# Optimization experiments

Hardware: AMD Instinct MI355X
Metric: run time of the kernel (lower is better)

Reference implementation:

```python
import jax, jax.numpy as jnp
import numpy as np

B, TI, TO = 32, 128, 64
VI, VO = 32000, 32000
E, H, A = 256, 512, 512
EOS, BOS = 0, 1


def setup_inputs() -> dict:
    key = jax.random.key(0)
    ks = jax.random.split(key, 24)
    def p(k, shape):
        return jax.random.normal(k, shape, jnp.float32) * 0.05
    return {
        "inp": jax.random.randint(ks[0], (B, TI), 0, VI),
        "out": jax.random.randint(ks[1], (B, TO), 0, VO),
        "emb_inp": p(ks[2], (VI, E)),
        "emb_out": p(ks[3], (VO, E)),
        "enc_Wih_f": p(ks[4], (3 * H, E)),
        "enc_Whh_f": p(ks[5], (3 * H, H)),
        "enc_bih_f": p(ks[6], (3 * H,)),
        "enc_bhh_f": p(ks[7], (3 * H,)),
        "enc_Wih_b": p(ks[8], (3 * H, E)),
        "enc_Whh_b": p(ks[9], (3 * H, H)),
        "enc_bih_b": p(ks[10], (3 * H,)),
        "enc_bhh_b": p(ks[11], (3 * H,)),
        "dec_start_W": p(ks[12], (H, 2 * H)),
        "dec_start_b": p(ks[13], (H,)),
        "dec_Wih": p(ks[14], (3 * H, E + 2 * H)),
        "dec_Whh": p(ks[15], (3 * H, H)),
        "dec_bih": p(ks[16], (3 * H,)),
        "dec_bhh": p(ks[17], (3 * H,)),
        "attn_Wenc": p(ks[18], (A, 2 * H)),
        "attn_benc": p(ks[19], (A,)),
        "attn_Wdec": p(ks[20], (A, H)),
        "attn_bdec": p(ks[21], (A,)),
        "attn_v": p(ks[22], (A,)),
        "attn_vb": jnp.zeros((), jnp.float32),
        "logits_W": p(ks[23], (VO, 3 * H)),
        "logits_b": jnp.zeros((VO,), jnp.float32),
    }


def _gru_dir(x, Wih, bih, Whh, bhh, reverse):
    # x: [B,T,E]; precompute input projections once: [B,T,3H]
    xp = jnp.einsum('bte,ge->btg', x, Wih) + bih
    Hd = Whh.shape[1]
    def step(h, xt):
        gh = h @ Whh.T + bhh
        xr, xz, xn = jnp.split(xt, 3, -1)
        hr, hz, hn = jnp.split(gh, 3, -1)
        r = jax.nn.sigmoid(xr + hr)
        z = jax.nn.sigmoid(xz + hz)
        n = jnp.tanh(xn + r * hn)
        h_new = (1.0 - z) * n + z * h
        return h_new, h_new
    h0 = jnp.zeros((x.shape[0], Hd), x.dtype)
    _, hs = jax.lax.scan(step, h0, jnp.swapaxes(xp, 0, 1), reverse=reverse)
    return jnp.swapaxes(hs, 0, 1)  # [B,T,H]


def _forward(inp, out, emb_inp, emb_out,
             enc_Wih_f, enc_Whh_f, enc_bih_f, enc_bhh_f,
             enc_Wih_b, enc_Whh_b, enc_bih_b, enc_bhh_b,
             dec_start_W, dec_start_b, dec_Wih, dec_Whh, dec_bih, dec_bhh,
             attn_Wenc, attn_benc, attn_Wdec, attn_bdec, attn_v, attn_vb,
             logits_W, logits_b):
    x = emb_inp[inp]  # [B,TI,E]
    ef = _gru_dir(x, enc_Wih_f, enc_bih_f, enc_Whh_f, enc_bhh_f, False)
    eb = _gru_dir(x, enc_Wih_b, enc_bih_b, enc_Whh_b, enc_bhh_b, True)
    enc = jnp.concatenate([ef, eb], -1)  # [B,TI,2H]
    mask = (inp != EOS).astype(jnp.float32)
    lengths = jnp.minimum(mask.sum(1).astype(jnp.int32), TI - 1)
    last = enc[jnp.arange(enc.shape[0]), lengths]  # [B,2H]
    dec0 = last @ dec_start_W.T + dec_start_b  # [B,H]
    enc_proj = jnp.einsum('btd,ad->bta', enc, attn_Wenc) + attn_benc  # [B,TI,A]

    def attend(dec):
        dp = dec @ attn_Wdec.T + attn_bdec  # [B,A]
        s = jnp.tanh(enc_proj + dp[:, None, :]) @ attn_v + attn_vb  # [B,TI]
        s = jnp.where(mask > 0, s, -jnp.inf)
        pr = jax.nn.softmax(s, -1)
        return jnp.einsum('bt,btd->bd', pr, enc), pr

    a0, _ = attend(dec0)

    def step(carry, tok):
        h, a = carry
        e = emb_out[tok]  # [B,E]
        xg = jnp.concatenate([e, a], -1) @ dec_Wih.T + dec_bih
        hg = h @ dec_Whh.T + dec_bhh
        xr, xz, xn = jnp.split(xg, 3, -1)
        hr, hz, hn = jnp.split(hg, 3, -1)
        r = jax.nn.sigmoid(xr + hr)
        z = jax.nn.sigmoid(xz + hz)
        n = jnp.tanh(xn + r * hn)
        h_new = (1.0 - z) * n + z * h
        a_new, _ = attend(h_new)
        lg = jnp.concatenate([h_new, a_new], -1) @ logits_W.T + logits_b
        return (h_new, a_new), lg

    toks = jnp.swapaxes(out[:, :-1], 0, 1)  # [TO-1, B]
    _, lgs = jax.lax.scan(step, (dec0, a0), toks)  # [TO-1,B,VO]
    first = jnp.log(jax.nn.one_hot(jnp.full((out.shape[0],), BOS), VO) + 1e-9)
    return jnp.swapaxes(jnp.concatenate([first[None], lgs], 0), 0, 1)  # [B,TO,VO]


def reference(inp, out, emb_inp, emb_out,
              enc_Wih_f, enc_Whh_f, enc_bih_f, enc_bhh_f,
              enc_Wih_b, enc_Whh_b, enc_bih_b, enc_bhh_b,
              dec_start_W, dec_start_b, dec_Wih, dec_Whh, dec_bih, dec_bhh,
              attn_Wenc, attn_benc, attn_Wdec, attn_bdec, attn_v, attn_vb,
              logits_W, logits_b):
    return _forward(inp, out, emb_inp, emb_out,
                    enc_Wih_f, enc_Whh_f, enc_bih_f, enc_bhh_f,
                    enc_Wih_b, enc_Whh_b, enc_bih_b, enc_bhh_b,
                    dec_start_W, dec_start_b, dec_Wih, dec_Whh, dec_bih, dec_bhh,
                    attn_Wenc, attn_benc, attn_Wdec, attn_bdec, attn_v, attn_vb,
                    logits_W, logits_b)
```

## Files before the change

kernel.cpp:

```cpp
#include <hip/hip_runtime.h>
#include <math.h>
#include <stdint.h>

#define B_   32
#define TI_  128
#define TO_  64
#define E_   256
#define H_   512
#define A_   512
#define VO_  32000
#define G3_  1536
#define D2H_ 1024

using short8 = __attribute__((ext_vector_type(8))) short;
using f32x4  = __attribute__((ext_vector_type(4))) float;
typedef __attribute__((ext_vector_type(2))) __bf16 bf16x2_t;

__device__ __forceinline__ unsigned short f2bf(float x) {
  uint32_t u = __builtin_bit_cast(uint32_t, x);
  uint32_t r = (u + 0x7fffu + ((u >> 16) & 1u)) >> 16;
  return (unsigned short)r;
}
__device__ __forceinline__ uint32_t pack2(float lo, float hi) {
  return (uint32_t)f2bf(lo) | ((uint32_t)f2bf(hi) << 16);
}
__device__ __forceinline__ float bflo(uint32_t u) { return __builtin_bit_cast(float, u << 16); }
__device__ __forceinline__ float bfhi(uint32_t u) { return __builtin_bit_cast(float, u & 0xffff0000u); }

#if __has_builtin(__builtin_amdgcn_fdot2_f32_bf16)
__device__ __forceinline__ float dot2bf(uint32_t a, uint32_t b, float c) {
  return __builtin_amdgcn_fdot2_f32_bf16(__builtin_bit_cast(bf16x2_t, a),
                                         __builtin_bit_cast(bf16x2_t, b), c, false);
}
#else
__device__ __forceinline__ float dot2bf(uint32_t a, uint32_t b, float c) {
  return fmaf(bfhi(a), bfhi(b), fmaf(bflo(a), bflo(b), c));
}
#endif

__device__ __forceinline__ float sigf(float x) {
  return __builtin_amdgcn_rcpf(1.f + __expf(-x));
}
__device__ __forceinline__ float tanhf_(float x) {
  return fmaf(-2.f, __builtin_amdgcn_rcpf(1.f + __expf(2.f * x)), 1.f);
}

__global__ __launch_bounds__(256) void k_init(unsigned short* __restrict__ tail) {
  int i = blockIdx.x * 256 + threadIdx.x;
  if (i < 32 * G3_) tail[i] = 0;
}

__global__ __launch_bounds__(256) void k_cvt_bf16(const float* __restrict__ in,
                                                  unsigned short* __restrict__ out, int n8) {
  int i = blockIdx.x * 256 + threadIdx.x;
  if (i >= n8) return;
  float4 a = ((const float4*)in)[2 * i];
  float4 b = ((const float4*)in)[2 * i + 1];
  uint4 o = { pack2(a.x, a.y), pack2(a.z, a.w), pack2(b.x, b.y), pack2(b.z, b.w) };
  ((uint4*)out)[i] = o;
}

__global__ __launch_bounds__(256) void k_cvt_multi(
    const float* __restrict__ i0, unsigned short* __restrict__ o0,
    const float* __restrict__ i1, unsigned short* __restrict__ o1,
    const float* __restrict__ i2, unsigned short* __restrict__ o2,
    const float* __restrict__ i3, unsigned short* __restrict__ o3) {
  int u = blockIdx.x * 256 + threadIdx.x;
  const float* in; unsigned short* out; int lu;
  if      (u < 245760) { in = i0; out = o0; lu = u; }
  else if (u < 311296) { in = i1; out = o1; lu = u - 245760; }
  else if (u < 360448) { in = i2; out = o2; lu = u - 311296; }
  else if (u < 409600) { in = i3; out = o3; lu = u - 360448; }
  else return;
  float4 a = ((const float4*)in)[2 * lu];
  float4 b = ((const float4*)in)[2 * lu + 1];
  uint4 o = { pack2(a.x, a.y), pack2(a.z, a.w), pack2(b.x, b.y), pack2(b.z, b.w) };
  ((uint4*)out)[lu] = o;
}

__global__ __launch_bounds__(256) void k_cvt_tp(
    const float* __restrict__ i0, uint32_t* __restrict__ o0,
    const float* __restrict__ i1, uint32_t* __restrict__ o1,
    const float* __restrict__ i2, uint32_t* __restrict__ o2,
    const float* __restrict__ i3, uint32_t* __restrict__ o3) {
  int u = blockIdx.x * 256 + threadIdx.x;
  const float* in; uint32_t* out; int lu, N;
  if      (u < 393216)  { in = i0; out = o0; lu = u;          N = 1536; }
  else if (u < 786432)  { in = i1; out = o1; lu = u - 393216; N = 1536; }
  else if (u < 1179648) { in = i2; out = o2; lu = u - 786432; N = 1536; }
  else if (u < 1310720) { in = i3; out = o3; lu = u - 1179648; N = 512; }
  else return;
  int c = lu % N, kp = lu / N;
  const float* p = in + (size_t)c * 512 + 2 * kp;
  out[lu] = pack2(p[0], p[1]);
}

__global__ __launch_bounds__(256) void k_packT(const unsigned short* __restrict__ encWA,
                                               uint32_t* __restrict__ EWPd) {
  int idx = blockIdx.x * 256 + threadIdx.x;
  if (idx >= 32 * 64 * 1536) return;
  int g = idx % 1536, q = idx / 1536;
  int b = q >> 6, tp = q & 63;
  size_t r0 = ((size_t)(b * 128 + 2 * tp)) * 1536 + g;
  EWPd[idx] = (uint32_t)encWA[r0] | ((uint32_t)encWA[r0 + 1536] << 16);
}

__global__ __launch_bounds__(256) void k_gather_xb(const int* __restrict__ inp,
                                                   const float* __restrict__ emb,
                                                   unsigned short* __restrict__ xb) {
  int idx = blockIdx.x * 256 + threadIdx.x;
  if (idx >= 4096 * 32) return;
  int row = idx >> 5, e8 = idx & 31;
  int tok = inp[row];
  const float4* s = (const float4*)(emb + (size_t)tok * E_ + e8 * 8);
  float4 a = s[0], b = s[1];
  uint4 o = { pack2(a.x, a.y), pack2(a.z, a.w), pack2(b.x, b.y), pack2(b.z, b.w) };
  ((uint4*)xb)[idx] = o;
}

__global__ __launch_bounds__(256) void k_gather_xeb(const int* __restrict__ outi,
                                                    const float* __restrict__ emb,
                                                    unsigned short* __restrict__ xeb) {
  int idx = blockIdx.x * 256 + threadIdx.x;
  if (idx >= 2016 * 32) return;
  int row = idx >> 5, e8 = idx & 31;
  int i = row >> 5, b = row & 31;
  int tok = outi[b * TO_ + i];
  const float4* s = (const float4*)(emb + (size_t)tok * E_ + e8 * 8);
  float4 a = s[0], bb = s[1];
  uint4 o = { pack2(a.x, a.y), pack2(a.z, a.w), pack2(bb.x, bb.y), pack2(bb.z, bb.w) };
  ((uint4*)xeb)[idx] = o;
}

__global__ __launch_bounds__(256) void k_first(float* __restrict__ dout) {
  int idx = blockIdx.x * 256 + threadIdx.x;
  if (idx >= B_ * VO_) return;
  int b = idx / VO_, v = idx % VO_;
  dout[(size_t)b * TO_ * VO_ + v] = (v == 1) ? 0.f : -20.72326583694641f;
}

template <int MODE>
__global__ __launch_bounds__(256) void k_bgemm(
    const unsigned short* __restrict__ A, int lda,
    const unsigned short* __restrict__ Bt, int ldb,
    const float* __restrict__ bias,
    void* __restrict__ Cv, int ldc, int M, int N, int K) {
  __shared__ alignas(16) unsigned short As[128 * 32];
  __shared__ alignas(16) unsigned short Bs[128 * 32];
  const int tid = threadIdx.x;
  const int wave = tid >> 6, lane = tid & 63;
  const int m0 = blockIdx.y * 128, n0 = blockIdx.x * 128;
  const int wr = wave >> 1, wc = wave & 1;

  f32x4 acc[4][4];
#pragma unroll
  for (int i = 0; i < 4; ++i)
#pragma unroll
    for (int j = 0; j < 4; ++j) acc[i][j] = (f32x4){0.f, 0.f, 0.f, 0.f};

  const int srow = tid >> 2;
  const int sbyte = (tid & 3) * 16;
  const int fr = lane & 15;
  const int fkb = (lane >> 4) * 16;

  for (int k0 = 0; k0 < K; k0 += 32) {
#pragma unroll
    for (int rd = 0; rd < 2; ++rd) {
      int row = rd * 64 + srow;
      int ra = min(m0 + row, M - 1);
      const char* ga = (const char*)(A + (size_t)ra * lda + k0) + sbyte;
      const char* gb = (const char*)(Bt + (size_t)(n0 + row) * ldb + k0) + sbyte;
      __builtin_amdgcn_global_load_lds(
          (const __attribute__((address_space(1))) uint32_t*)ga,
          (__attribute__((address_space(3))) uint32_t*)((char*)As + rd * 4096 + wave * 1024),
          16, 0, 0);
      __builtin_amdgcn_global_load_lds(
          (const __attribute__((address_space(1))) uint32_t*)gb,
          (__attribute__((address_space(3))) uint32_t*)((char*)Bs + rd * 4096 + wave * 1024),
          16, 0, 0);
    }
    __syncthreads();

    short8 af[4], bf[4];
#pragma unroll
    for (int i = 0; i < 4; ++i) {
      int ar = wr * 64 + i * 16 + fr;
      int bc = wc * 64 + i * 16 + fr;
      af[i] = *(const short8*)((const char*)As + ar * 64 + fkb);
      bf[i] = *(const short8*)((const char*)Bs + bc * 64 + fkb);
    }
#pragma unroll
    for (int i = 0; i < 4; ++i)
#pragma unroll
      for (int j = 0; j < 4; ++j)
        acc[i][j] = __builtin_amdgcn_mfma_f32_16x16x32_bf16(af[i], bf[j], acc[i][j], 0, 0, 0);
    __syncthreads();
  }

  const int crow = (lane >> 4) * 4, ccol = lane & 15;
#pragma unroll
  for (int i = 0; i < 4; ++i) {
#pragma unroll
    for (int r = 0; r < 4; ++r) {
      int m = m0 + wr * 64 + i * 16 + crow + r;
      if (m >= M) continue;
#pragma unroll
      for (int j = 0; j < 4; ++j) {
        int n = n0 + wc * 64 + j * 16 + ccol;
        float v = acc[i][j][r] + (bias ? bias[n] : 0.f);
        if (MODE == 0) {
          ((float*)Cv)[(size_t)m * ldc + n] = v;
        } else if (MODE == 1) {
          ((unsigned short*)Cv)[(size_t)m * ldc + n] = f2bf(v);
        } else {
          int bb = m & 31, st = m >> 5;
          ((float*)Cv)[((size_t)bb * TO_ + st + 1) * VO_ + n] = v;
        }
      }
    }
  }
}

__global__ __launch_bounds__(1024, 4) void k_encoder(
    const unsigned short* __restrict__ xpb_f, const unsigned short* __restrict__ xpb_b,
    const uint32_t* __restrict__ EWPf, const float* __restrict__ bhh_f,
    const uint32_t* __restrict__ EWPb, const float* __restrict__ bhh_b,
    unsigned short* __restrict__ encb) {
  __shared__ uint32_t xrow[768];
  __shared__ float hf[512];
  __shared__ uint32_t hb2[256];
  const int bid = blockIdx.x;
  const int dir = bid >> 5, b = bid & 31;
  const unsigned short* xpb = dir ? xpb_b : xpb_f;
  const uint32_t* EWP = dir ? EWPb : EWPf;
  const float* bhh = dir ? bhh_b : bhh_f;
  const int tid = threadIdx.x;
  const int col = tid >> 1, kh = tid & 1;

  if (tid < 512) hf[tid] = 0.f;
  if (tid < 256) hb2[tid] = 0u;
  float br = 0.f, bz = 0.f, bn = 0.f;
  if (kh == 0) { br = bhh[col]; bz = bhh[512 + col]; bn = bhh[1024 + col]; }
  uint32_t* encw = (uint32_t*)encb;

  for (int t = 0; t < TI_; ++t) {
    const int tt = dir ? (TI_ - 1 - t) : t;
    const uint32_t* xr = (const uint32_t*)(xpb + (size_t)(b * 128 + tt) * G3_);
    if (tid < 768) xrow[tid] = xr[tid];
    __syncthreads();

    float ar = 0.f, az = 0.f, an = 0.f;
    const uint32_t* wp = EWP + (size_t)(kh * 128) * 1536 + col;
#pragma unroll 8
    for (int k = 0; k < 128; ++k) {
      uint32_t hv = hb2[kh * 128 + k];
      ar = dot2bf(hv, wp[0], ar);
      az = dot2bf(hv, wp[512], az);
      an = dot2bf(hv, wp[1024], an);
      wp += 1536;
    }
    ar += __shfl_xor(ar, 1);
    az += __shfl_xor(az, 1);
    an += __shfl_xor(an, 1);

    float hnew = 0.f;
    if (kh == 0) {
      uint32_t ur = xrow[col >> 1], uz = xrow[256 + (col >> 1)], un = xrow[512 + (col >> 1)];
      float xrv = (col & 1) ? bfhi(ur) : bflo(ur);
      float xzv = (col & 1) ? bfhi(uz) : bflo(uz);
      float xnv = (col & 1) ? bfhi(un) : bflo(un);
      float r = sigf(xrv + ar + br);
      float z = sigf(xzv + az + bz);
      float n = tanhf_(xnv + r * (an + bn));
      hnew = (1.f - z) * n + z * hf[col];
    }
    __syncthreads();
    float hnb = __shfl_down(hnew, 2);
    if ((tid & 3) == 0)
      encw[(size_t)(b * 128 + tt) * 512 + dir * 256 + (tid >> 2)] = pack2(hnew, hnb);
    if (kh == 0) hf[col] = hnew;
    __syncthreads();
    if (tid < 256) hb2[tid] = pack2(hf[2 * tid], hf[2 * tid + 1]);
    __syncthreads();
  }
}

__global__ __launch_bounds__(1024, 4) void k_decoder(
    const int* __restrict__ inp,
    const unsigned short* __restrict__ encb,
    const unsigned short* __restrict__ encpb,
    const float* __restrict__ XE,
    const uint32_t* __restrict__ EWPd,
    const uint32_t* __restrict__ WHPd,
    const uint32_t* __restrict__ WDPd,
    const float* __restrict__ dsW, const float* __restrict__ dsb,
    const float* __restrict__ dbhh,
    const float* __restrict__ abdec, const float* __restrict__ abenc,
    const float* __restrict__ av, const float* __restrict__ avb,
    unsigned short* __restrict__ HAb) {
  __shared__ float hf[512];
  __shared__ uint32_t hb2[256];
  __shared__ uint32_t prb2[64];
  __shared__ float pr[128];
  __shared__ float sc[128];
  __shared__ float msk[128];
  __shared__ float dp[512];
  __shared__ float vavf[512];
  __shared__ float red[1024];
  __shared__ float red2[1024];
  __shared__ float dpx[4];
  const int b = blockIdx.x, tid = threadIdx.x;
  const int col = tid >> 1, kh = tid & 1;

  float db_r = 0.f, db_z = 0.f, db_n = 0.f, adb = 0.f;
  if (kh == 0) {
    db_r = dbhh[col]; db_z = dbhh[512 + col]; db_n = dbhh[1024 + col];
    adb = abdec[col] + abenc[col];
  }
  const float avb0 = avb[0];

  if (tid < 128) msk[tid] = (inp[b * TI_ + tid] != 0) ? 1.f : 0.f;
  if (tid < 512) vavf[tid] = av[tid];
  __syncthreads();
  if (tid < 64) {
    float s = msk[tid] + msk[tid + 64];
#pragma unroll
    for (int o = 32; o > 0; o >>= 1) s += __shfl_xor(s, o);
    if (tid == 0) dpx[0] = s;
  }
  __syncthreads();
  const int len = min((int)dpx[0], TI_ - 1);

  if (tid < 512) {
    uint32_t u = ((const uint32_t*)encb)[(size_t)(b * 128 + len) * 512 + tid];
    red[2 * tid] = bflo(u);
    red[2 * tid + 1] = bfhi(u);
  }
  __syncthreads();
  {
    const float4* w = (const float4*)(dsW + (size_t)col * D2H_ + kh * 512);
    float acc = 0.f;
#pragma unroll 8
    for (int k = 0; k < 128; ++k) {
      float4 l = ((const float4*)red)[kh * 128 + k];
      float4 q = w[k];
      acc = fmaf(l.x, q.x, fmaf(l.y, q.y, fmaf(l.z, q.z, fmaf(l.w, q.w, acc))));
    }
    acc += __shfl_xor(acc, 1);
    __syncthreads();
    if (kh == 0) hf[col] = acc + dsb[col];
    __syncthreads();
    if (tid < 256) hb2[tid] = pack2(hf[2 * tid], hf[2 * tid + 1]);
    __syncthreads();
  }

  auto attend = [&](int step) {
    {
      const uint32_t* wp = WDPd + (size_t)(kh * 128) * 512 + col;
      float d_ = 0.f;
#pragma unroll 8
      for (int k = 0; k < 128; ++k) {
        d_ = dot2bf(hb2[kh * 128 + k], wp[0], d_);
        wp += 512;
      }
      d_ += __shfl_xor(d_, 1);
      if (kh == 0) dp[col] = d_ + adb;
    }
    __syncthreads();
    {
      int t = tid >> 3, s8 = tid & 7;
      const uint32_t* ep = (const uint32_t*)encpb + (size_t)(b * 128 + t) * 256 + s8;
      float s = 0.f;
#pragma unroll 4
      for (int i = 0; i < 32; ++i) {
        int j = s8 + 8 * i;
        uint32_t u = ep[8 * i];
        float2 d2 = *(const float2*)&dp[2 * j];
        float2 v2 = *(const float2*)&vavf[2 * j];
        s = fmaf(v2.x, tanhf_(bflo(u) + d2.x), s);
        s = fmaf(v2.y, tanhf_(bfhi(u) + d2.y), s);
      }
      s += __shfl_xor(s, 1);
      s += __shfl_xor(s, 2);
      s += __shfl_xor(s, 4);
      if (s8 == 0) sc[t] = s;
    }
    __syncthreads();
    if (tid < 128) sc[tid] = (msk[tid] > 0.f) ? sc[tid] + avb0 : -1e30f;
    __syncthreads();
    if (tid < 64) {
      float m = fmaxf(sc[tid], sc[tid + 64]);
#pragma unroll
      for (int o = 32; o > 0; o >>= 1) m = fmaxf(m, __shfl_xor(m, o));
      if (tid == 0) dpx[1] = m;
    }
    __syncthreads();
    if (tid < 128) pr[tid] = __expf(sc[tid] - dpx[1]);
    __syncthreads();
    if (tid < 64) {
      float s2 = pr[tid] + pr[tid + 64];
#pragma unroll
      for (int o = 32; o > 0; o >>= 1) s2 += __shfl_xor(s2, o);
      if (tid == 0) dpx[2] = s2;
    }
    __syncthreads();
    float inv = __builtin_amdgcn_rcpf(dpx[2]);
    if (tid < 128) pr[tid] *= inv;
    __syncthreads();
    if (tid < 64) prb2[tid] = pack2(pr[2 * tid], pr[2 * tid + 1]);
    if (step >= 0) {
      const uint32_t* eb = (const uint32_t*)encb + (size_t)b * 128 * 512;
      int d = tid & 511, tq = tid >> 9;
      float x0 = 0.f, x1 = 0.f;
#pragma unroll 4
      for (int k = 0; k < 64; ++k) {
        int t = tq * 64 + k;
        float p = pr[t];
        uint32_t u = eb[(size_t)t * 512 + d];
        x0 = fmaf(p, bflo(u), x0);
        x1 = fmaf(p, bfhi(u), x1);
      }
      red[tid] = x0; red2[tid] = x1;
      __syncthreads();
      if (tid < 512) {
        x0 = red[tid] + red[tid + 512];
        x1 = red2[tid] + red2[tid + 512];
        uint32_t* hrow = (uint32_t*)(HAb + ((size_t)step * 32 + b) * G3_);
        hrow[256 + tid] = pack2(x0, x1);
      }
    }
    __syncthreads();
  };

  auto gru = [&](int i) {
    float xr_ = 0.f, xz_ = 0.f, xn_ = 0.f, hr_ = 0.f, hz_ = 0.f, hn_ = 0.f;
    {
      const uint32_t* ew = EWPd + ((size_t)b * 64 + kh * 32) * 1536 + col;
#pragma unroll 8
      for (int k = 0; k < 32; ++k) {
        uint32_t pv = prb2[kh * 32 + k];
        xr_ = dot2bf(pv, ew[0], xr_);
        xz_ = dot2bf(pv, ew[512], xz_);
        xn_ = dot2bf(pv, ew[1024], xn_);
        ew += 1536;
      }
    }
    {
      const uint32_t* wp = WHPd + (size_t)(kh * 128) * 1536 + col;
#pragma unroll 8
      for (int k = 0; k < 128; ++k) {
        uint32_t hv = hb2[kh * 128 + k];
        hr_ = dot2bf(hv, wp[0], hr_);
        hz_ = dot2bf(hv, wp[512], hz_);
        hn_ = dot2bf(hv, wp[1024], hn_);
        wp += 1536;
      }
    }
    float t_r = xr_ + hr_; t_r += __shfl_xor(t_r, 1);
    float t_z = xz_ + hz_; t_z += __shfl_xor(t_z, 1);
    xn_ += __shfl_xor(xn_, 1);
    hn_ += __shfl_xor(hn_, 1);

    float hnew = 0.f;
    if (kh == 0) {
      const float* xrow = XE + ((size_t)i * 32 + b) * G3_;
      float r = sigf(xrow[col] + t_r + db_r);
      float z = sigf(xrow[512 + col] + t_z + db_z);
      float n = tanhf_(xrow[1024 + col] + xn_ + r * (hn_ + db_n));
      hnew = (1.f - z) * n + z * hf[col];
    }
    __syncthreads();
    float hnb = __shfl_down(hnew, 2);
    if ((tid & 3) == 0)
      ((uint32_t*)(HAb + ((size_t)i * 32 + b) * G3_))[tid >> 2] = pack2(hnew, hnb);
    if (kh == 0) hf[col] = hnew;
    __syncthreads();
    if (tid < 256) hb2[tid] = pack2(hf[2 * tid], hf[2 * tid + 1]);
    __syncthreads();
  };

  attend(-1);
  for (int i = 0; i < 63; ++i) {
    gru(i);
    attend(i);
  }
}


extern "C" void kernel_launch(void* const* d_in, const int* in_sizes, int n_in,
                              void* d_out, int out_size, void* d_ws, size_t ws_size,
                              hipStream_t stream) {
  const int*   inp     = (const int*)d_in[0];
  const int*   outi    = (const int*)d_in[1];
  const float* emb_inp = (const float*)d_in[2];
  const float* emb_out = (const float*)d_in[3];
  const float* eWih_f  = (const float*)d_in[4];
  const float* eWhh_f  = (const float*)d_in[5];
  const float* ebih_f  = (const float*)d_in[6];
  const float* ebhh_f  = (const float*)d_in[7];
  const float* eWih_b  = (const float*)d_in[8];
  const float* eWhh_b  = (const float*)d_in[9];
  const float* ebih_b  = (const float*)d_in[10];
  const float* ebhh_b  = (const float*)d_in[11];
  const float* dsW     = (const float*)d_in[12];
  const float* dsb     = (const float*)d_in[13];
  const float* dWih    = (const float*)d_in[14];
  const float* dWhh    = (const float*)d_in[15];
  const float* dbih    = (const float*)d_in[16];
  const float* dbhh    = (const float*)d_in[17];
  const float* aWenc   = (const float*)d_in[18];
  const float* abenc   = (const float*)d_in[19];
  const float* aWdec   = (const float*)d_in[20];
  const float* abdec   = (const float*)d_in[21];
  const float* av      = (const float*)d_in[22];
  const float* avb     = (const float*)d_in[23];
  const float* lW      = (const float*)d_in[24];
  const float* lb      = (const float*)d_in[25];
  float* dout = (float*)d_out;

  char* ws = (char*)d_ws;
  size_t off = 0;
  auto alloc = [&](size_t bytes) {
    void* p = ws + off;
    off += (bytes + 255) & ~(size_t)255;
    return p;
  };
  unsigned short* xb      = (unsigned short*)alloc((size_t)4096 * 256 * 2);
  unsigned short* xeb     = (unsigned short*)alloc((size_t)2016 * 256 * 2);
  unsigned short* xpb_f   = (unsigned short*)alloc((size_t)4096 * G3_ * 2);
  unsigned short* xpb_b   = (unsigned short*)alloc((size_t)4096 * G3_ * 2);
  unsigned short* encb    = (unsigned short*)alloc((size_t)4096 * D2H_ * 2);
  unsigned short* encpb   = (unsigned short*)alloc((size_t)4096 * 512 * 2);
  unsigned short* encWA   = (unsigned short*)alloc((size_t)4096 * G3_ * 2);
  uint32_t*       EWPd    = (uint32_t*)alloc((size_t)32 * 64 * 1536 * 4);
  float*          XE      = (float*)alloc((size_t)2016 * G3_ * 4);
  unsigned short* HAb     = (unsigned short*)alloc((size_t)2048 * G3_ * 2);
  unsigned short* lWb     = (unsigned short*)alloc((size_t)VO_ * G3_ * 2);
  uint32_t*       EWPf    = (uint32_t*)alloc((size_t)256 * 1536 * 4);
  uint32_t*       EWPb    = (uint32_t*)alloc((size_t)256 * 1536 * 4);
  uint32_t*       WHPd    = (uint32_t*)alloc((size_t)256 * 1536 * 4);
  uint32_t*       WDPd    = (uint32_t*)alloc((size_t)256 * 512 * 4);
  unsigned short* dWihb   = (unsigned short*)alloc((size_t)G3_ * 1280 * 2);
  unsigned short* aWencb  = (unsigned short*)alloc((size_t)512 * D2H_ * 2);
  unsigned short* eWihb_f = (unsigned short*)alloc((size_t)G3_ * 256 * 2);
  unsigned short* eWihb_b = (unsigned short*)alloc((size_t)G3_ * 256 * 2);

  k_init<<<192, 256, 0, stream>>>(HAb + (size_t)2016 * G3_);
  k_cvt_multi<<<1600, 256, 0, stream>>>(dWih, dWihb, aWenc, aWencb,
                                        eWih_f, eWihb_f, eWih_b, eWihb_b);
  k_cvt_tp<<<5120, 256, 0, stream>>>(eWhh_f, EWPf, eWhh_b, EWPb, dWhh, WHPd, aWdec, WDPd);
  k_cvt_bf16<<<24000, 256, 0, stream>>>(lW, lWb, VO_ * G3_ / 8);

  k_gather_xb<<<512, 256, 0, stream>>>(inp, emb_inp, xb);
  k_gather_xeb<<<252, 256, 0, stream>>>(outi, emb_out, xeb);

  {
    dim3 g(12, 32);
    k_bgemm<1><<<g, 256, 0, stream>>>(xb, 256, eWihb_f, 256, ebih_f, xpb_f, G3_, 4096, G3_, 256);
    k_bgemm<1><<<g, 256, 0, stream>>>(xb, 256, eWihb_b, 256, ebih_b, xpb_b, G3_, 4096, G3_, 256);
  }

  k_encoder<<<64, 1024, 0, stream>>>(xpb_f, xpb_b, EWPf, ebhh_f, EWPb, ebhh_b, encb);

  {
    dim3 g(4, 32);
    k_bgemm<1><<<g, 256, 0, stream>>>(encb, D2H_, aWencb, D2H_, nullptr, encpb, 512, 4096, 512, D2H_);
  }
  {
    dim3 g(12, 32);
    k_bgemm<1><<<g, 256, 0, stream>>>(encb, D2H_, dWihb + 256, 1280, nullptr, encWA, G3_, 4096, G3_, D2H_);
  }
  k_packT<<<12288, 256, 0, stream>>>(encWA, EWPd);

  {
    dim3 g(12, 16);
    k_bgemm<0><<<g, 256, 0, stream>>>(xeb, 256, dWihb, 1280, dbih, XE, G3_, 2016, G3_, 256);
  }

  k_decoder<<<32, 1024, 0, stream>>>(inp, encb, encpb, XE, EWPd, WHPd, WDPd,
                                     dsW, dsb, dbhh, abdec, abenc, av, avb, HAb);

  {
    dim3 g(250, 16);
    k_bgemm<3><<<g, 256, 0, stream>>>(HAb, G3_, lWb, G3_, lb, dout, 0, 2016, VO_, G3_);
  }
  k_first<<<4000, 256, 0, stream>>>(dout);
}
```

Measured before the change: 11.10 ms.

## Repack recurrent GRU weights as column pairs with 4-way k-split and register prefetch

Recurrent weight matrices for the encoder and decoder (Whh, attention Wdec, and the per-batch encoder-attention projection) are repacked so each uint2 holds two output columns for a k-pair. Each thread now computes two columns over a quarter of k, with double-buffered register prefetch of weight loads. The hidden state is kept in padded shared memory, so the separate bf16 repack pass and one barrier per step are dropped. The aim is wider global loads and better latency hiding in the latency-bound sequential loops, at the cost of more registers and an extra shuffle reduction stage.

```diff
diff --git a/kernel.cpp b/kernel.cpp
--- a/kernel.cpp
+++ b/kernel.cpp
@@ -78,31 +78,41 @@
   ((uint4*)out)[lu] = o;
 }
 
-__global__ __launch_bounds__(256) void k_cvt_tp(
-    const float* __restrict__ i0, uint32_t* __restrict__ o0,
-    const float* __restrict__ i1, uint32_t* __restrict__ o1,
-    const float* __restrict__ i2, uint32_t* __restrict__ o2,
-    const float* __restrict__ i3, uint32_t* __restrict__ o3) {
+__global__ __launch_bounds__(256) void k_cvt_w2(
+    const float* __restrict__ i0, uint2* __restrict__ o0,
+    const float* __restrict__ i1, uint2* __restrict__ o1,
+    const float* __restrict__ i2, uint2* __restrict__ o2,
+    const float* __restrict__ i3, uint2* __restrict__ o3) {
   int u = blockIdx.x * 256 + threadIdx.x;
-  const float* in; uint32_t* out; int lu, N;
-  if      (u < 393216)  { in = i0; out = o0; lu = u;          N = 1536; }
-  else if (u < 786432)  { in = i1; out = o1; lu = u - 393216; N = 1536; }
-  else if (u < 1179648) { in = i2; out = o2; lu = u - 786432; N = 1536; }
-  else if (u < 1310720) { in = i3; out = o3; lu = u - 1179648; N = 512; }
+  const float* in; uint2* out; int lu, perkp;
+  if      (u < 196608) { in = i0; out = o0; lu = u;          perkp = 768; }
+  else if (u < 393216) { in = i1; out = o1; lu = u - 196608; perkp = 768; }
+  else if (u < 589824) { in = i2; out = o2; lu = u - 393216; perkp = 768; }
+  else if (u < 655360) { in = i3; out = o3; lu = u - 589824; perkp = 256; }
   else return;
-  int c = lu % N, kp = lu / N;
-  const float* p = in + (size_t)c * 512 + 2 * kp;
-  out[lu] = pack2(p[0], p[1]);
-}
-
-__global__ __launch_bounds__(256) void k_packT(const unsigned short* __restrict__ encWA,
-                                               uint32_t* __restrict__ EWPd) {
+  int kp = lu / perkp, rest = lu % perkp;
+  int gg = rest >> 8, cg = rest & 255;
+  int row0 = gg * 512 + 2 * cg;
+  const float* p0 = in + (size_t)row0 * 512 + 2 * kp;
+  const float* p1 = p0 + 512;
+  uint2 o = { pack2(p0[0], p0[1]), pack2(p1[0], p1[1]) };
+  out[lu] = o;
+}
+
+__global__ __launch_bounds__(256) void k_packT2(const unsigned short* __restrict__ encWA,
+                                                uint2* __restrict__ EW2) {
   int idx = blockIdx.x * 256 + threadIdx.x;
-  if (idx >= 32 * 64 * 1536) return;
-  int g = idx % 1536, q = idx / 1536;
-  int b = q >> 6, tp = q & 63;
-  size_t r0 = ((size_t)(b * 128 + 2 * tp)) * 1536 + g;
-  EWPd[idx] = (uint32_t)encWA[r0] | ((uint32_t)encWA[r0 + 1536] << 16);
+  if (idx >= 32 * 64 * 768) return;
+  int rest = idx % 768, q = idx / 768;
+  int tp = q & 63, b = q >> 6;
+  int gg = rest >> 8, cg = rest & 255;
+  int col0 = gg * 512 + 2 * cg;
+  size_t r0 = ((size_t)(b * 128 + 2 * tp)) * 1536;
+  size_t r1 = r0 + 1536;
+  uint2 o;
+  o.x = (uint32_t)encWA[r0 + col0] | ((uint32_t)encWA[r1 + col0] << 16);
+  o.y = (uint32_t)encWA[r0 + col0 + 1] | ((uint32_t)encWA[r1 + col0 + 1] << 16);
+  EW2[idx] = o;
 }
 
 __global__ __launch_bounds__(256) void k_gather_xb(const int* __restrict__ inp,
@@ -223,64 +233,96 @@
 
 __global__ __launch_bounds__(1024, 4) void k_encoder(
     const unsigned short* __restrict__ xpb_f, const unsigned short* __restrict__ xpb_b,
-    const uint32_t* __restrict__ EWPf, const float* __restrict__ bhh_f,
-    const uint32_t* __restrict__ EWPb, const float* __restrict__ bhh_b,
+    const uint2* __restrict__ W2f, const float* __restrict__ bhh_f,
+    const uint2* __restrict__ W2b, const float* __restrict__ bhh_b,
     unsigned short* __restrict__ encb) {
-  __shared__ uint32_t xrow[768];
+  __shared__ uint32_t hb2p[260];
   __shared__ float hf[512];
-  __shared__ uint32_t hb2[256];
   const int bid = blockIdx.x;
   const int dir = bid >> 5, b = bid & 31;
   const unsigned short* xpb = dir ? xpb_b : xpb_f;
-  const uint32_t* EWP = dir ? EWPb : EWPf;
+  const uint2* W2 = dir ? W2b : W2f;
   const float* bhh = dir ? bhh_b : bhh_f;
   const int tid = threadIdx.x;
-  const int col = tid >> 1, kh = tid & 1;
+  const int cg = tid >> 2, kq = tid & 3;
+  const int c0 = 2 * cg, c1 = c0 + 1;
 
   if (tid < 512) hf[tid] = 0.f;
-  if (tid < 256) hb2[tid] = 0u;
-  float br = 0.f, bz = 0.f, bn = 0.f;
-  if (kh == 0) { br = bhh[col]; bz = bhh[512 + col]; bn = bhh[1024 + col]; }
+  if (tid < 260) hb2p[tid] = 0u;
+  float br0 = 0, br1 = 0, bz0 = 0, bz1 = 0, bn0 = 0, bn1 = 0;
+  if (kq == 0) {
+    br0 = bhh[c0]; br1 = bhh[c1];
+    bz0 = bhh[512 + c0]; bz1 = bhh[512 + c1];
+    bn0 = bhh[1024 + c0]; bn1 = bhh[1024 + c1];
+  }
+  const uint2* wbase = W2 + (size_t)(kq * 64) * 768 + cg;
+  const uint32_t* hq = hb2p + kq * 65;
   uint32_t* encw = (uint32_t*)encb;
+  __syncthreads();
 
   for (int t = 0; t < TI_; ++t) {
     const int tt = dir ? (TI_ - 1 - t) : t;
-    const uint32_t* xr = (const uint32_t*)(xpb + (size_t)(b * 128 + tt) * G3_);
-    if (tid < 768) xrow[tid] = xr[tid];
-    __syncthreads();
-
-    float ar = 0.f, az = 0.f, an = 0.f;
-    const uint32_t* wp = EWP + (size_t)(kh * 128) * 1536 + col;
-#pragma unroll 8
-    for (int k = 0; k < 128; ++k) {
-      uint32_t hv = hb2[kh * 128 + k];
-      ar = dot2bf(hv, wp[0], ar);
-      az = dot2bf(hv, wp[512], az);
-      an = dot2bf(hv, wp[1024], an);
-      wp += 1536;
-    }
-    ar += __shfl_xor(ar, 1);
-    az += __shfl_xor(az, 1);
-    an += __shfl_xor(an, 1);
-
-    float hnew = 0.f;
-    if (kh == 0) {
-      uint32_t ur = xrow[col >> 1], uz = xrow[256 + (col >> 1)], un = xrow[512 + (col >> 1)];
-      float xrv = (col & 1) ? bfhi(ur) : bflo(ur);
-      float xzv = (col & 1) ? bfhi(uz) : bflo(uz);
-      float xnv = (col & 1) ? bfhi(un) : bflo(un);
-      float r = sigf(xrv + ar + br);
-      float z = sigf(xzv + az + bz);
-      float n = tanhf_(xnv + r * (an + bn));
-      hnew = (1.f - z) * n + z * hf[col];
-    }
-    __syncthreads();
-    float hnb = __shfl_down(hnew, 2);
-    if ((tid & 3) == 0)
-      encw[(size_t)(b * 128 + tt) * 512 + dir * 256 + (tid >> 2)] = pack2(hnew, hnb);
-    if (kh == 0) hf[col] = hnew;
-    __syncthreads();
-    if (tid < 256) hb2[tid] = pack2(hf[2 * tid], hf[2 * tid + 1]);
+    float ar0 = 0, ar1 = 0, az0 = 0, az1 = 0, an0 = 0, an1 = 0;
+    {
+      const uint2* wp = wbase;
+      uint2 buf[2][3][4];
+#pragma unroll
+      for (int j = 0; j < 4; ++j) {
+        buf[0][0][j] = wp[(size_t)j * 768];
+        buf[0][1][j] = wp[(size_t)j * 768 + 256];
+        buf[0][2][j] = wp[(size_t)j * 768 + 512];
+      }
+      wp += 4 * 768;
+#pragma unroll
+      for (int c = 0; c < 16; ++c) {
+        const int cur = c & 1, nxt = cur ^ 1;
+        if (c < 15) {
+#pragma unroll
+          for (int j = 0; j < 4; ++j) {
+            buf[nxt][0][j] = wp[(size_t)j * 768];
+            buf[nxt][1][j] = wp[(size_t)j * 768 + 256];
+            buf[nxt][2][j] = wp[(size_t)j * 768 + 512];
+          }
+          wp += 4 * 768;
+        }
+#pragma unroll
+        for (int j = 0; j < 4; ++j) {
+          uint32_t hv = hq[c * 4 + j];
+          ar0 = dot2bf(hv, buf[cur][0][j].x, ar0);
+          ar1 = dot2bf(hv, buf[cur][0][j].y, ar1);
+          az0 = dot2bf(hv, buf[cur][1][j].x, az0);
+          az1 = dot2bf(hv, buf[cur][1][j].y, az1);
+          an0 = dot2bf(hv, buf[cur][2][j].x, an0);
+          an1 = dot2bf(hv, buf[cur][2][j].y, an1);
+        }
+      }
+    }
+    ar0 += __shfl_xor(ar0, 1); ar0 += __shfl_xor(ar0, 2);
+    ar1 += __shfl_xor(ar1, 1); ar1 += __shfl_xor(ar1, 2);
+    az0 += __shfl_xor(az0, 1); az0 += __shfl_xor(az0, 2);
+    az1 += __shfl_xor(az1, 1); az1 += __shfl_xor(az1, 2);
+    an0 += __shfl_xor(an0, 1); an0 += __shfl_xor(an0, 2);
+    an1 += __shfl_xor(an1, 1); an1 += __shfl_xor(an1, 2);
+
+    float hn0 = 0.f, hn1 = 0.f;
+    if (kq == 0) {
+      const uint32_t* xr = (const uint32_t*)(xpb + (size_t)(b * 128 + tt) * G3_);
+      uint32_t uxr = xr[cg], uxz = xr[256 + cg], uxn = xr[512 + cg];
+      float r0 = sigf(bflo(uxr) + ar0 + br0);
+      float r1 = sigf(bfhi(uxr) + ar1 + br1);
+      float z0 = sigf(bflo(uxz) + az0 + bz0);
+      float z1 = sigf(bfhi(uxz) + az1 + bz1);
+      float n0 = tanhf_(bflo(uxn) + r0 * (an0 + bn0));
+      float n1 = tanhf_(bfhi(uxn) + r1 * (an1 + bn1));
+      hn0 = (1.f - z0) * n0 + z0 * hf[c0];
+      hn1 = (1.f - z1) * n1 + z1 * hf[c1];
+      encw[(size_t)(b * 128 + tt) * 512 + dir * 256 + cg] = pack2(hn0, hn1);
+    }
+    __syncthreads();
+    if (kq == 0) {
+      hf[c0] = hn0; hf[c1] = hn1;
+      hb2p[cg + (cg >> 6)] = pack2(hn0, hn1);
+    }
     __syncthreads();
   }
 }
@@ -290,16 +332,16 @@
     const unsigned short* __restrict__ encb,
     const unsigned short* __restrict__ encpb,
     const float* __restrict__ XE,
-    const uint32_t* __restrict__ EWPd,
-    const uint32_t* __restrict__ WHPd,
-    const uint32_t* __restrict__ WDPd,
+    const uint2* __restrict__ EW2,
+    const uint2* __restrict__ WH2,
+    const uint2* __restrict__ WD2,
     const float* __restrict__ dsW, const float* __restrict__ dsb,
     const float* __restrict__ dbhh,
     const float* __restrict__ abdec, const float* __restrict__ abenc,
     const float* __restrict__ av, const float* __restrict__ avb,
     unsigned short* __restrict__ HAb) {
+  __shared__ uint32_t hb2p[260];
   __shared__ float hf[512];
-  __shared__ uint32_t hb2[256];
   __shared__ uint32_t prb2[64];
   __shared__ float pr[128];
   __shared__ float sc[128];
@@ -310,12 +352,18 @@
   __shared__ float red2[1024];
   __shared__ float dpx[4];
   const int b = blockIdx.x, tid = threadIdx.x;
-  const int col = tid >> 1, kh = tid & 1;
-
-  float db_r = 0.f, db_z = 0.f, db_n = 0.f, adb = 0.f;
-  if (kh == 0) {
-    db_r = dbhh[col]; db_z = dbhh[512 + col]; db_n = dbhh[1024 + col];
-    adb = abdec[col] + abenc[col];
+  const int cg = tid >> 2, kq = tid & 3;
+  const int c0 = 2 * cg, c1 = c0 + 1;
+  const uint32_t* hq = hb2p + kq * 65;
+
+  float db_r0 = 0, db_r1 = 0, db_z0 = 0, db_z1 = 0, db_n0 = 0, db_n1 = 0;
+  float adb0 = 0, adb1 = 0;
+  if (kq == 0) {
+    db_r0 = dbhh[c0]; db_r1 = dbhh[c1];
+    db_z0 = dbhh[512 + c0]; db_z1 = dbhh[512 + c1];
+    db_n0 = dbhh[1024 + c0]; db_n1 = dbhh[1024 + c1];
+    adb0 = abdec[c0] + abenc[c0];
+    adb1 = abdec[c1] + abenc[c1];
   }
   const float avb0 = avb[0];
 
@@ -338,6 +386,7 @@
   }
   __syncthreads();
   {
+    const int col = tid >> 1, kh = tid & 1;
     const float4* w = (const float4*)(dsW + (size_t)col * D2H_ + kh * 512);
     float acc = 0.f;
 #pragma unroll 8
@@ -350,21 +399,36 @@
     __syncthreads();
     if (kh == 0) hf[col] = acc + dsb[col];
     __syncthreads();
-    if (tid < 256) hb2[tid] = pack2(hf[2 * tid], hf[2 * tid + 1]);
+    if (tid < 256) hb2p[tid + (tid >> 6)] = pack2(hf[2 * tid], hf[2 * tid + 1]);
     __syncthreads();
   }
 
   auto attend = [&](int step) {
     {
-      const uint32_t* wp = WDPd + (size_t)(kh * 128) * 512 + col;
-      float d_ = 0.f;
-#pragma unroll 8
-      for (int k = 0; k < 128; ++k) {
-        d_ = dot2bf(hb2[kh * 128 + k], wp[0], d_);
-        wp += 512;
-      }
-      d_ += __shfl_xor(d_, 1);
-      if (kh == 0) dp[col] = d_ + adb;
+      const uint2* wp = WD2 + (size_t)(kq * 64) * 256 + cg;
+      float d0 = 0.f, d1 = 0.f;
+      uint2 bufd[2][4];
+#pragma unroll
+      for (int j = 0; j < 4; ++j) bufd[0][j] = wp[(size_t)j * 256];
+      wp += 4 * 256;
+#pragma unroll
+      for (int c = 0; c < 16; ++c) {
+        const int cur = c & 1, nxt = cur ^ 1;
+        if (c < 15) {
+#pragma unroll
+          for (int j = 0; j < 4; ++j) bufd[nxt][j] = wp[(size_t)j * 256];
+          wp += 4 * 256;
+        }
+#pragma unroll
+        for (int j = 0; j < 4; ++j) {
+          uint32_t hv = hq[c * 4 + j];
+          d0 = dot2bf(hv, bufd[cur][j].x, d0);
+          d1 = dot2bf(hv, bufd[cur][j].y, d1);
+        }
+      }
+      d0 += __shfl_xor(d0, 1); d0 += __shfl_xor(d0, 2);
+      d1 += __shfl_xor(d1, 1); d1 += __shfl_xor(d1, 2);
+      if (kq == 0) { dp[c0] = d0 + adb0; dp[c1] = d1 + adb1; }
     }
     __syncthreads();
     {
@@ -433,49 +497,103 @@
   };
 
   auto gru = [&](int i) {
-    float xr_ = 0.f, xz_ = 0.f, xn_ = 0.f, hr_ = 0.f, hz_ = 0.f, hn_ = 0.f;
+    float xr0 = 0, xr1 = 0, xz0 = 0, xz1 = 0, xn0 = 0, xn1 = 0;
     {
-      const uint32_t* ew = EWPd + ((size_t)b * 64 + kh * 32) * 1536 + col;
-#pragma unroll 8
-      for (int k = 0; k < 32; ++k) {
-        uint32_t pv = prb2[kh * 32 + k];
-        xr_ = dot2bf(pv, ew[0], xr_);
-        xz_ = dot2bf(pv, ew[512], xz_);
-        xn_ = dot2bf(pv, ew[1024], xn_);
-        ew += 1536;
-      }
-    }
+      const uint2* ep = EW2 + ((size_t)b * 64 + kq * 16) * 768 + cg;
+      uint2 bufe[2][3][2];
+#pragma unroll
+      for (int j = 0; j < 2; ++j) {
+        bufe[0][0][j] = ep[(size_t)j * 768];
+        bufe[0][1][j] = ep[(size_t)j * 768 + 256];
+        bufe[0][2][j] = ep[(size_t)j * 768 + 512];
+      }
+      ep += 2 * 768;
+#pragma unroll
+      for (int c = 0; c < 8; ++c) {
+        const int cur = c & 1, nxt = cur ^ 1;
+        if (c < 7) {
+#pragma unroll
+          for (int j = 0; j < 2; ++j) {
+            bufe[nxt][0][j] = ep[(size_t)j * 768];
+            bufe[nxt][1][j] = ep[(size_t)j * 768 + 256];
+            bufe[nxt][2][j] = ep[(size_t)j * 768 + 512];
+          }
+          ep += 2 * 768;
+        }
+#pragma unroll
+        for (int j = 0; j < 2; ++j) {
+          uint32_t pv = prb2[kq * 16 + c * 2 + j];
+          xr0 = dot2bf(pv, bufe[cur][0][j].x, xr0);
+          xr1 = dot2bf(pv, bufe[cur][0][j].y, xr1);
+          xz0 = dot2bf(pv, bufe[cur][1][j].x, xz0);
+          xz1 = dot2bf(pv, bufe[cur][1][j].y, xz1);
+          xn0 = dot2bf(pv, bufe[cur][2][j].x, xn0);
+          xn1 = dot2bf(pv, bufe[cur][2][j].y, xn1);
+        }
+      }
+    }
+    float hr0 = 0, hr1 = 0, hz0 = 0, hz1 = 0, hn0_ = 0, hn1_ = 0;
     {
-      const uint32_t* wp = WHPd + (size_t)(kh * 128) * 1536 + col;
-#pragma unroll 8
-      for (int k = 0; k < 128; ++k) {
-        uint32_t hv = hb2[kh * 128 + k];
-        hr_ = dot2bf(hv, wp[0], hr_);
-        hz_ = dot2bf(hv, wp[512], hz_);
-        hn_ = dot2bf(hv, wp[1024], hn_);
-        wp += 1536;
-      }
-    }
-    float t_r = xr_ + hr_; t_r += __shfl_xor(t_r, 1);
-    float t_z = xz_ + hz_; t_z += __shfl_xor(t_z, 1);
-    xn_ += __shfl_xor(xn_, 1);
-    hn_ += __shfl_xor(hn_, 1);
-
-    float hnew = 0.f;
-    if (kh == 0) {
+      const uint2* wp = WH2 + (size_t)(kq * 64) * 768 + cg;
+      uint2 buf[2][3][4];
+#pragma unroll
+      for (int j = 0; j < 4; ++j) {
+        buf[0][0][j] = wp[(size_t)j * 768];
+        buf[0][1][j] = wp[(size_t)j * 768 + 256];
+        buf[0][2][j] = wp[(size_t)j * 768 + 512];
+      }
+      wp += 4 * 768;
+#pragma unroll
+      for (int c = 0; c < 16; ++c) {
+        const int cur = c & 1, nxt = cur ^ 1;
+        if (c < 15) {
+#pragma unroll
+          for (int j = 0; j < 4; ++j) {
+            buf[nxt][0][j] = wp[(size_t)j * 768];
+            buf[nxt][1][j] = wp[(size_t)j * 768 + 256];
+            buf[nxt][2][j] = wp[(size_t)j * 768 + 512];
+          }
+          wp += 4 * 768;
+        }
+#pragma unroll
+        for (int j = 0; j < 4; ++j) {
+          uint32_t hv = hq[c * 4 + j];
+          hr0 = dot2bf(hv, buf[cur][0][j].x, hr0);
+          hr1 = dot2bf(hv, buf[cur][0][j].y, hr1);
+          hz0 = dot2bf(hv, buf[cur][1][j].x, hz0);
+          hz1 = dot2bf(hv, buf[cur][1][j].y, hz1);
+          hn0_ = dot2bf(hv, buf[cur][2][j].x, hn0_);
+          hn1_ = dot2bf(hv, buf[cur][2][j].y, hn1_);
+        }
+      }
+    }
+    float tr0 = xr0 + hr0; tr0 += __shfl_xor(tr0, 1); tr0 += __shfl_xor(tr0, 2);
+    float tr1 = xr1 + hr1; tr1 += __shfl_xor(tr1, 1); tr1 += __shfl_xor(tr1, 2);
+    float tz0 = xz0 + hz0; tz0 += __shfl_xor(tz0, 1); tz0 += __shfl_xor(tz0, 2);
+    float tz1 = xz1 + hz1; tz1 += __shfl_xor(tz1, 1); tz1 += __shfl_xor(tz1, 2);
+    xn0 += __shfl_xor(xn0, 1); xn0 += __shfl_xor(xn0, 2);
+    xn1 += __shfl_xor(xn1, 1); xn1 += __shfl_xor(xn1, 2);
+    hn0_ += __shfl_xor(hn0_, 1); hn0_ += __shfl_xor(hn0_, 2);
+    hn1_ += __shfl_xor(hn1_, 1); hn1_ += __shfl_xor(hn1_, 2);
+
+    float hnew0 = 0.f, hnew1 = 0.f;
+    if (kq == 0) {
       const float* xrow = XE + ((size_t)i * 32 + b) * G3_;
-      float r = sigf(xrow[col] + t_r + db_r);
-      float z = sigf(xrow[512 + col] + t_z + db_z);
-      float n = tanhf_(xrow[1024 + col] + xn_ + r * (hn_ + db_n));
-      hnew = (1.f - z) * n + z * hf[col];
-    }
-    __syncthreads();
-    float hnb = __shfl_down(hnew, 2);
-    if ((tid & 3) == 0)
-      ((uint32_t*)(HAb + ((size_t)i * 32 + b) * G3_))[tid >> 2] = pack2(hnew, hnb);
-    if (kh == 0) hf[col] = hnew;
-    __syncthreads();
-    if (tid < 256) hb2[tid] = pack2(hf[2 * tid], hf[2 * tid + 1]);
+      float r0 = sigf(xrow[c0] + tr0 + db_r0);
+      float r1 = sigf(xrow[c1] + tr1 + db_r1);
+      float z0 = sigf(xrow[512 + c0] + tz0 + db_z0);
+      float z1 = sigf(xrow[512 + c1] + tz1 + db_z1);
+      float n0 = tanhf_(xrow[1024 + c0] + xn0 + r0 * (hn0_ + db_n0));
+      float n1 = tanhf_(xrow[1024 + c1] + xn1 + r1 * (hn1_ + db_n1));
+      hnew0 = (1.f - z0) * n0 + z0 * hf[c0];
+      hnew1 = (1.f - z1) * n1 + z1 * hf[c1];
+      ((uint32_t*)(HAb + ((size_t)i * 32 + b) * G3_))[cg] = pack2(hnew0, hnew1);
+    }
+    __syncthreads();
+    if (kq == 0) {
+      hf[c0] = hnew0; hf[c1] = hnew1;
+      hb2p[cg + (cg >> 6)] = pack2(hnew0, hnew1);
+    }
     __syncthreads();
   };
 
@@ -532,14 +650,14 @@
   unsigned short* encb    = (unsigned short*)alloc((size_t)4096 * D2H_ * 2);
   unsigned short* encpb   = (unsigned short*)alloc((size_t)4096 * 512 * 2);
   unsigned short* encWA   = (unsigned short*)alloc((size_t)4096 * G3_ * 2);
-  uint32_t*       EWPd    = (uint32_t*)alloc((size_t)32 * 64 * 1536 * 4);
+  uint2*          EW2d    = (uint2*)alloc((size_t)32 * 64 * 768 * 8);
   float*          XE      = (float*)alloc((size_t)2016 * G3_ * 4);
   unsigned short* HAb     = (unsigned short*)alloc((size_t)2048 * G3_ * 2);
   unsigned short* lWb     = (unsigned short*)alloc((size_t)VO_ * G3_ * 2);
-  uint32_t*       EWPf    = (uint32_t*)alloc((size_t)256 * 1536 * 4);
-  uint32_t*       EWPb    = (uint32_t*)alloc((size_t)256 * 1536 * 4);
-  uint32_t*       WHPd    = (uint32_t*)alloc((size_t)256 * 1536 * 4);
-  uint32_t*       WDPd    = (uint32_t*)alloc((size_t)256 * 512 * 4);
+  uint2*          W2f     = (uint2*)alloc((size_t)196608 * 8);
+  uint2*          W2b     = (uint2*)alloc((size_t)196608 * 8);
+  uint2*          WH2     = (uint2*)alloc((size_t)196608 * 8);
+  uint2*          WD2     = (uint2*)alloc((size_t)65536 * 8);
   unsigned short* dWihb   = (unsigned short*)alloc((size_t)G3_ * 1280 * 2);
   unsigned short* aWencb  = (unsigned short*)alloc((size_t)512 * D2H_ * 2);
   unsigned short* eWihb_f = (unsigned short*)alloc((size_t)G3_ * 256 * 2);
@@ -548,7 +666,7 @@
   k_init<<<192, 256, 0, stream>>>(HAb + (size_t)2016 * G3_);
   k_cvt_multi<<<1600, 256, 0, stream>>>(dWih, dWihb, aWenc, aWencb,
                                         eWih_f, eWihb_f, eWih_b, eWihb_b);
-  k_cvt_tp<<<5120, 256, 0, stream>>>(eWhh_f, EWPf, eWhh_b, EWPb, dWhh, WHPd, aWdec, WDPd);
+  k_cvt_w2<<<2560, 256, 0, stream>>>(eWhh_f, W2f, eWhh_b, W2b, dWhh, WH2, aWdec, WD2);
   k_cvt_bf16<<<24000, 256, 0, stream>>>(lW, lWb, VO_ * G3_ / 8);
 
   k_gather_xb<<<512, 256, 0, stream>>>(inp, emb_inp, xb);
@@ -560,7 +678,7 @@
     k_bgemm<1><<<g, 256, 0, stream>>>(xb, 256, eWihb_b, 256, ebih_b, xpb_b, G3_, 4096, G3_, 256);
   }
 
-  k_encoder<<<64, 1024, 0, stream>>>(xpb_f, xpb_b, EWPf, ebhh_f, EWPb, ebhh_b, encb);
+  k_encoder<<<64, 1024, 0, stream>>>(xpb_f, xpb_b, W2f, ebhh_f, W2b, ebhh_b, encb);
 
   {
     dim3 g(4, 32);
@@ -570,14 +688,14 @@
     dim3 g(12, 32);
     k_bgemm<1><<<g, 256, 0, stream>>>(encb, D2H_, dWihb + 256, 1280, nullptr, encWA, G3_, 4096, G3_, D2H_);
   }
-  k_packT<<<12288, 256, 0, stream>>>(encWA, EWPd);
+  k_packT2<<<6144, 256, 0, stream>>>(encWA, EW2d);
 
   {
     dim3 g(12, 16);
     k_bgemm<0><<<g, 256, 0, stream>>>(xeb, 256, dWihb, 1280, dbih, XE, G3_, 2016, G3_, 256);
   }
 
-  k_decoder<<<32, 1024, 0, stream>>>(inp, encb, encpb, XE, EWPd, WHPd, WDPd,
+  k_decoder<<<32, 1024, 0, stream>>>(inp, encb, encpb, XE, EW2d, WH2, WD2,
                                      dsW, dsb, dbhh, abdec, abenc, av, avb, HAb);
 
   {
```

Measured after the change: 13.73 ms. 23.7% more time.
